# Kernel optimization log

Hardware: AMD Instinct MI355X
Metric: run time of the kernel (lower is better)

## Reference

```python
import jax, jax.numpy as jnp
import numpy as np

E = 1024      # embed_dim
H = 16        # num_heads
HD = E // H   # head_dim = 64
WIN = 256     # window_size
LN_EPS = 1e-5


def _layernorm(x, g, b):
    mu = jnp.mean(x, axis=-1, keepdims=True)
    var = jnp.var(x, axis=-1, keepdims=True)
    return (x - mu) * jax.lax.rsqrt(var + LN_EPS) * g + b


def _rope_tables(S):
    freqs = 1.0 / (10000.0 ** (jnp.arange(0, HD, 2, dtype=jnp.float32) / HD))  # [HD/2]
    t = jnp.arange(S, dtype=jnp.float32)
    fr = jnp.outer(t, freqs)                      # [S, HD/2]
    emb = jnp.concatenate([fr, fr], axis=-1)      # [S, HD]
    # shape [S, 1, HD] so it broadcasts over the heads dim of [B, S, H, HD]
    return emb[:, None, :].astype(jnp.float32), None


def _rotate_half(x):
    x1, x2 = jnp.split(x, 2, axis=-1)
    return jnp.concatenate([-x2, x1], axis=-1)


def setup_inputs() -> dict:
    key = jax.random.key(0)
    ks = jax.random.split(key, 12)
    B, S = 8, 1024
    sc = 0.02
    return {
        "x": jax.random.normal(ks[0], (B, S, E), dtype=jnp.float32),
        "in_proj_w": jax.random.normal(ks[1], (3 * E, E), dtype=jnp.float32) * sc,
        "in_proj_b": jnp.zeros((3 * E,), dtype=jnp.float32),
        "out_proj_w": jax.random.normal(ks[2], (E, E), dtype=jnp.float32) * sc,
        "out_proj_b": jnp.zeros((E,), dtype=jnp.float32),
        "ln1_g": jnp.ones((E,), dtype=jnp.float32),
        "ln1_b": jnp.zeros((E,), dtype=jnp.float32),
        "w1": jax.random.normal(ks[3], (4 * E, E), dtype=jnp.float32) * sc,
        "b1": jnp.zeros((4 * E,), dtype=jnp.float32),
        "w2": jax.random.normal(ks[4], (E, 4 * E), dtype=jnp.float32) * sc,
        "b2": jnp.zeros((E,), dtype=jnp.float32),
        "ln2_g": jnp.ones((E,), dtype=jnp.float32),
        "ln2_b": jnp.zeros((E,), dtype=jnp.float32),
    }


def reference(x, in_proj_w, in_proj_b, out_proj_w, out_proj_b,
              ln1_g, ln1_b, w1, b1, w2, b2, ln2_g, ln2_b):
    B, S, _ = x.shape
    # RoPE applied to the raw input (pre in_proj), as in the torch module
    emb, _ = _rope_tables(S)
    cos, sin = jnp.cos(emb), jnp.sin(emb)          # [S, 1, HD]
    xh = x.reshape(B, S, H, HD)
    roped = xh * cos + _rotate_half(xh) * sin      # [B, S, H, HD]
    qk_in = roped.reshape(B, S, E)

    Wq, Wk, Wv = jnp.split(in_proj_w, 3, axis=0)   # each [E, E]
    bq, bk, bv = jnp.split(in_proj_b, 3, axis=0)
    q = (qk_in @ Wq.T + bq).reshape(B, S, H, HD).transpose(0, 2, 1, 3)  # [B,H,S,HD]
    k = (qk_in @ Wk.T + bk).reshape(B, S, H, HD).transpose(0, 2, 1, 3)
    v = (x @ Wv.T + bv).reshape(B, S, H, HD).transpose(0, 2, 1, 3)

    scale = 1.0 / np.sqrt(HD)
    scores = jnp.einsum("bhqd,bhkd->bhqk", q, k) * scale  # [B,H,S,S]
    idx = jnp.arange(S)
    disallowed = jnp.abs(idx[:, None] - idx[None, :]) > WIN  # [S,S] bool
    scores = jnp.where(disallowed, jnp.float32(-jnp.inf), scores)
    attn = jax.nn.softmax(scores, axis=-1)
    ctx = jnp.einsum("bhqk,bhkd->bhqd", attn, v)            # [B,H,S,HD]
    ctx = ctx.transpose(0, 2, 1, 3).reshape(B, S, E)
    h = ctx @ out_proj_w.T + out_proj_b

    x1 = _layernorm(x + h, ln1_g, ln1_b)
    ff = jax.nn.gelu(x1 @ w1.T + b1, approximate=False) @ w2.T + b2
    return _layernorm(x1 + ff, ln2_g, ln2_b)
```

## Files before the change

kernel.cpp:

```cpp
#include <hip/hip_runtime.h>
#include <stdint.h>


#define B_ 8
#define S_ 1024
#define E_ 1024
#define H_ 16
#define HD_ 64
#define WIN_ 256
#define QKV_ 3072

typedef __attribute__((ext_vector_type(8))) short short8;
typedef __attribute__((ext_vector_type(4))) float f32x4;
typedef __attribute__((ext_vector_type(4))) unsigned short us4;
typedef unsigned short ushort_t;

__device__ __forceinline__ ushort_t f2b(float f) {
  unsigned int u = __builtin_bit_cast(unsigned int, f);
  u = (u + 0x7fffu + ((u >> 16) & 1u)) >> 16;
  return (ushort_t)u;
}

__device__ __forceinline__ ushort_t f2b_trunc(float f) {
  return (ushort_t)(__builtin_bit_cast(unsigned int, f) >> 16);
}

__device__ __forceinline__ float b2f(ushort_t u) {
  return __builtin_bit_cast(float, ((unsigned int)u) << 16);
}

__device__ __forceinline__ float fast_exp2(float x) {
#if __has_builtin(__builtin_amdgcn_exp2f)
  return __builtin_amdgcn_exp2f(x);
#else
  return exp2f(x);
#endif
}

__device__ __forceinline__ float fast_rcp(float x) {
#if __has_builtin(__builtin_amdgcn_rcpf)
  return __builtin_amdgcn_rcpf(x);
#else
  return 1.f / x;
#endif
}

__device__ __forceinline__ void gld_lds16(const void* g, void* l) {
  __builtin_amdgcn_global_load_lds((const __attribute__((address_space(1))) void*)g,
                                   (__attribute__((address_space(3))) void*)l, 16, 0, 0);
}

__global__ __launch_bounds__(256) void cast4_kernel(const float* __restrict__ i0,
                                                    const float* __restrict__ i1,
                                                    const float* __restrict__ i2,
                                                    const float* __restrict__ i3,
                                                    ushort_t* __restrict__ o0,
                                                    ushort_t* __restrict__ o1,
                                                    ushort_t* __restrict__ o2,
                                                    ushort_t* __restrict__ o3) {
  int i = blockIdx.x * 256 + threadIdx.x;
  const float* in;
  ushort_t* out;
  int j;
  if (i < 786432)       { in = i0; out = o0; j = i; }
  else if (i < 1048576) { in = i1; out = o1; j = i - 786432; }
  else if (i < 2097152) { in = i2; out = o2; j = i - 1048576; }
  else                  { in = i3; out = o3; j = i - 2097152; }
  float4 v = ((const float4*)in)[j];
  us4 o;
  o.x = f2b(v.x); o.y = f2b(v.y); o.z = f2b(v.z); o.w = f2b(v.w);
  ((us4*)out)[j] = o;
}

__global__ __launch_bounds__(256) void rope_kernel(const float* __restrict__ x,
                                                   ushort_t* __restrict__ roped,
                                                   ushort_t* __restrict__ xbf) {
  int idx = blockIdx.x * 256 + threadIdx.x;
  int d = idx & 31;
  int h = (idx >> 5) & 15;
  int s = (idx >> 9) & 1023;
  int b = idx >> 19;
  size_t base = ((size_t)(b * S_ + s)) * E_ + h * HD_ + d;
  float x0 = x[base], x1 = x[base + 32];
  float freq = exp2f(-(float)d * 0.41524101186092029f);
  float th = (float)s * freq;
  float sn, cs;
  sincosf(th, &sn, &cs);
  roped[base]      = f2b(x0 * cs - x1 * sn);
  roped[base + 32] = f2b(x1 * cs + x0 * sn);
  xbf[base]      = f2b(x0);
  xbf[base + 32] = f2b(x1);
}

template <int MODE>
__global__ __launch_bounds__(256) void gemm_bt(const ushort_t* __restrict__ A,
                                               const ushort_t* __restrict__ A2,
                                               int nsplit,
                                               const ushort_t* __restrict__ Bm,
                                               const float* __restrict__ bias,
                                               ushort_t* __restrict__ C,
                                               int N, int K) {
  __shared__ ushort_t sA[128 * 64];
  __shared__ ushort_t sB[128 * 64];
  const int tid = threadIdx.x;
  const int lane = tid & 63;
  const int wave = tid >> 6;
  const int quad = lane >> 4;
  const int lq = lane & 15;
  const int wm = (wave & 1) * 64;
  const int wn = (wave >> 1) * 64;
  const size_t bm = (size_t)blockIdx.x * 128;
  const size_t bn = (size_t)blockIdx.y * 128;
  const ushort_t* Asel = (bn >= (size_t)nsplit) ? A2 : A;

  f32x4 acc[4][4] = {};

  const int srow = lane >> 3;
  const int skc = ((lane & 7) ^ (lane >> 3)) * 8;

  for (int k0 = 0; k0 < K; k0 += 64) {
#pragma unroll
    for (int i = 0; i < 4; i++) {
      const int r0 = wave * 32 + i * 8;
      gld_lds16(Asel + (bm + r0 + srow) * K + k0 + skc, &sA[r0 * 64]);
      gld_lds16(Bm + (bn + r0 + srow) * K + k0 + skc, &sB[r0 * 64]);
    }
    __syncthreads();

#pragma unroll
    for (int kk = 0; kk < 2; kk++) {
      const int csw = (((kk * 4) + quad) ^ (lq & 7)) * 8;
      short8 av[4], bv[4];
#pragma unroll
      for (int mt = 0; mt < 4; mt++)
        av[mt] = *(const short8*)&sA[(wm + mt * 16 + lq) * 64 + csw];
#pragma unroll
      for (int nt = 0; nt < 4; nt++)
        bv[nt] = *(const short8*)&sB[(wn + nt * 16 + lq) * 64 + csw];
#pragma unroll
      for (int mt = 0; mt < 4; mt++)
#pragma unroll
        for (int nt = 0; nt < 4; nt++)
          acc[mt][nt] = __builtin_amdgcn_mfma_f32_16x16x32_bf16(av[mt], bv[nt], acc[mt][nt], 0, 0, 0);
    }
    __syncthreads();
  }

#pragma unroll
  for (int mt = 0; mt < 4; mt++) {
#pragma unroll
    for (int nt = 0; nt < 4; nt++) {
      size_t row = bm + wm + mt * 16 + quad * 4;
      size_t col = bn + wn + nt * 16 + lq;
      float bc = bias[col];
#pragma unroll
      for (int r = 0; r < 4; r++) {
        float v = acc[mt][nt][r] + bc;
        if (MODE == 1) {
          float y = 0.7978845608028654f * (v + 0.044715f * v * v * v);
          float t = fast_exp2(y * 2.8853900817779268f);
          v = v * (t * fast_rcp(1.f + t));
        }
        C[(row + r) * N + col] = f2b(v);
      }
    }
  }
}

#define FENCE asm volatile("" ::: "memory")
#define VM6 asm volatile("s_waitcnt vmcnt(6)" ::: "memory")
#define VM0 asm volatile("s_waitcnt vmcnt(0)" ::: "memory")
#define NOPW ((void)0)

#define STAGE_A(bufc, half, kb)                                               \
  { gld_lds16(aSrc + (size_t)((half) * 128) * K + (kb),                       \
              &lds[16384 * (bufc) + 8192 * (half) + wave * 512]);             \
    gld_lds16(aSrc + (size_t)((half) * 128 + 64) * K + (kb),                  \
              &lds[16384 * (bufc) + 8192 * (half) + 4096 + wave * 512]); }

#define STAGE_B(bufc, half, kb)                                               \
  { gld_lds16(bSrc + (size_t)((half) * 128) * K + (kb),                       \
              &lds[32768 + 16384 * (bufc) + 8192 * (half) + wave * 512]);     \
    gld_lds16(bSrc + (size_t)((half) * 128 + 64) * K + (kb),                  \
              &lds[32768 + 16384 * (bufc) + 8192 * (half) + 4096 + wave * 512]); }

#define PHASE(qq, bufc, doA, doB, STAGE_STMT, WAIT_STMT)                      \
  {                                                                           \
    if (doA) {                                                                \
      const int abase = 16384 * (bufc) + 8192 * ((qq) >> 1);                  \
      _Pragma("unroll") for (int mf = 0; mf < 4; mf++) {                      \
        const int ra = wm * 64 + mf * 16 + lq;                                \
        _Pragma("unroll") for (int k2 = 0; k2 < 2; k2++)                      \
          av[mf][k2] = *(const short8*)&lds[abase + ra * 64 +                 \
                                            (((k2 * 4 + quad) ^ (lq & 7)) << 3)]; \
      }                                                                       \
    }                                                                         \
    if (doB) {                                                                \
      const int bbase = 32768 + 16384 * (bufc) +                              \
                        8192 * ((((qq) == 1) || ((qq) == 2)) ? 1 : 0);        \
      _Pragma("unroll") for (int nf = 0; nf < 2; nf++) {                      \
        const int rb = wn * 32 + nf * 16 + lq;                                \
        _Pragma("unroll") for (int k2 = 0; k2 < 2; k2++)                      \
          bv[nf][k2] = *(const short8*)&lds[bbase + rb * 64 +                 \
                                            (((k2 * 4 + quad) ^ (lq & 7)) << 3)]; \
      }                                                                       \
    }                                                                         \
    STAGE_STMT;                                                               \
    FENCE; __builtin_amdgcn_s_barrier(); FENCE;                               \
    __builtin_amdgcn_s_setprio(1);                                            \
    _Pragma("unroll") for (int k2 = 0; k2 < 2; k2++)                          \
      _Pragma("unroll") for (int mf = 0; mf < 4; mf++)                        \
        _Pragma("unroll") for (int nf = 0; nf < 2; nf++)                      \
          acc[qq][mf][nf] = __builtin_amdgcn_mfma_f32_16x16x32_bf16(          \
              av[mf][k2], bv[nf][k2], acc[qq][mf][nf], 0, 0, 0);              \
    __builtin_amdgcn_s_setprio(0);                                            \
    WAIT_STMT;                                                                \
    FENCE; __builtin_amdgcn_s_barrier(); FENCE;                               \
  }

template <int MODE>
__global__ __launch_bounds__(512, 2) void gemm256(const ushort_t* __restrict__ A,
                                                  const ushort_t* __restrict__ A2,
                                                  int nsplit,
                                                  const ushort_t* __restrict__ Bm,
                                                  const float* __restrict__ bias,
                                                  ushort_t* __restrict__ C,
                                                  int N, int K, int nbx) {
  __shared__ ushort_t lds[65536];
  const int tid = threadIdx.x;
  const int lane = tid & 63, wave = tid >> 6;
  const int quad = lane >> 4, lq = lane & 15;
  const int wm = wave >> 2, wn = wave & 3;

  const int nwg = gridDim.x;
  const int id = blockIdx.x;
  const int wg = (nwg & 7) ? id : ((id & 7) * (nwg >> 3) + (id >> 3));
  const int bx = wg % nbx, by = wg / nbx;
  const size_t bm = (size_t)bx * 256, bn = (size_t)by * 256;
  const ushort_t* Asel = ((int)bn >= nsplit) ? A2 : A;

  const int srow = lane >> 3;
  const int scol = ((lane & 7) ^ srow) << 3;
  const ushort_t* aSrc = Asel + (bm + wave * 8 + srow) * (size_t)K + scol;
  const ushort_t* bSrc = Bm + (bn + wave * 8 + srow) * (size_t)K + scol;

  f32x4 acc[4][4][2] = {};
  short8 av[4][2], bv[2][2];

  STAGE_A(0, 0, 0); STAGE_A(0, 1, 0); STAGE_B(0, 0, 0); STAGE_B(0, 1, 0);
  STAGE_A(1, 0, 64); STAGE_B(1, 1, 64); STAGE_A(1, 1, 64);
  VM6;
  FENCE; __builtin_amdgcn_s_barrier(); FENCE;

  const int NT = K >> 6;
#pragma unroll 1
  for (int i = 0; i < (NT >> 1) - 1; i++) {
    const int kb0 = i << 7;
    PHASE(0, 0, 1, 1, STAGE_B(1, 0, kb0 + 64), NOPW);
    PHASE(1, 0, 0, 1, STAGE_A(0, 0, kb0 + 128), NOPW);
    PHASE(2, 0, 1, 0, STAGE_B(0, 1, kb0 + 128), NOPW);
    PHASE(3, 0, 0, 1, STAGE_A(0, 1, kb0 + 128), VM6);
    PHASE(0, 1, 1, 1, STAGE_B(0, 0, kb0 + 128), NOPW);
    PHASE(1, 1, 0, 1, STAGE_A(1, 0, kb0 + 192), NOPW);
    PHASE(2, 1, 1, 0, STAGE_B(1, 1, kb0 + 192), NOPW);
    PHASE(3, 1, 0, 1, STAGE_A(1, 1, kb0 + 192), VM6);
  }
  {
    const int kb0 = (NT - 2) << 6;
    PHASE(0, 0, 1, 1, STAGE_B(1, 0, kb0 + 64), NOPW);
    PHASE(1, 0, 0, 1, NOPW, NOPW);
    PHASE(2, 0, 1, 0, NOPW, NOPW);
    PHASE(3, 0, 0, 1, NOPW, VM0);
    PHASE(0, 1, 1, 1, NOPW, NOPW);
    PHASE(1, 1, 0, 1, NOPW, NOPW);
    PHASE(2, 1, 1, 0, NOPW, NOPW);
    PHASE(3, 1, 0, 1, NOPW, NOPW);
  }

#pragma unroll
  for (int q = 0; q < 4; q++) {
    const int Mh = q >> 1;
    const int Nh = (q == 1 || q == 2) ? 1 : 0;
#pragma unroll
    for (int mf = 0; mf < 4; mf++) {
#pragma unroll
      for (int nf = 0; nf < 2; nf++) {
        size_t row = bm + Mh * 128 + wm * 64 + mf * 16 + quad * 4;
        size_t col = bn + Nh * 128 + wn * 32 + nf * 16 + lq;
        float bc = bias[col];
#pragma unroll
        for (int r = 0; r < 4; r++) {
          float v = acc[q][mf][nf][r] + bc;
          if (MODE == 1) {
            float y = 0.7978845608028654f * (v + 0.044715f * v * v * v);
            float t = fast_exp2(y * 2.8853900817779268f);
            v = v * (t * fast_rcp(1.f + t));
          }
          C[(row + r) * N + col] = f2b(v);
        }
      }
    }
  }
}

__global__ __launch_bounds__(256) void vtrans_kernel(const ushort_t* __restrict__ qkv,
                                                     ushort_t* __restrict__ vt) {
  __shared__ ushort_t tb[64 * 65];
  int bh = blockIdx.x >> 4;
  int st = blockIdx.x & 15;
  int b = bh >> 4, h = bh & 15;
  int s0 = st * 64;
  int tid = threadIdx.x;
  int c = tid & 63, rbase = tid >> 6;
#pragma unroll
  for (int rep = 0; rep < 16; rep++) {
    int i = rep * 4 + rbase;
    tb[c * 65 + i] = qkv[(size_t)(b * S_ + s0 + i) * QKV_ + 2048 + h * HD_ + c];
  }
  __syncthreads();
#pragma unroll
  for (int rep = 0; rep < 16; rep++) {
    int d = rep * 4 + rbase;
    vt[(size_t)((b * H_ + h) * HD_ + d) * S_ + s0 + c] = tb[d * 65 + c];
  }
}

#define SC_ 0.18033688011112042f

__global__ __launch_bounds__(256) void attn_kernel(const ushort_t* __restrict__ qkv,
                                                   const ushort_t* __restrict__ vt,
                                                   ushort_t* __restrict__ ctx) {
  __shared__ ushort_t sK[2][32 * 64];
  __shared__ ushort_t sV[2][64 * 32];
  __shared__ ushort_t sP[4][16 * 36];
  const int tid = threadIdx.x;
  const int lane = tid & 63, wave = tid >> 6;
  const int quad = lane >> 4, lq = lane & 15;
  int gid = ((blockIdx.x & 7) << 8) | (blockIdx.x >> 3);
  int qs = gid & 15;
  int h = (gid >> 4) & 15;
  int b = gid >> 8;
  int qs64 = qs * 64;
  int q0 = qs64 + wave * 16;

  const size_t qoff = (size_t)(b * S_ + q0 + lq) * QKV_ + h * HD_;
  short8 a0 = *(const short8*)&qkv[qoff + quad * 8];
  short8 a1 = *(const short8*)&qkv[qoff + 32 + quad * 8];

  f32x4 o[4] = {};
  float rs[4] = {0.f, 0.f, 0.f, 0.f};

  int start = qs64 - WIN_; if (start < 0) start = 0;
  int end = qs64 + 64 + WIN_; if (end > S_) end = S_;
  const int wlo = q0 - WIN_;
  const int whi = q0 + 16 + WIN_;

  const ushort_t* kg = qkv + (size_t)(b * S_) * QKV_ + 1024 + h * HD_;
  const ushort_t* vg = vt + (size_t)((b * H_ + h) * HD_) * S_;

  const int krow = lane >> 3;
  const int kchg = ((lane & 7) ^ krow) << 3;
  const int vrow = lane >> 2;
  const int vchg = ((lane & 3) ^ ((lane >> 3) & 3)) << 3;

  gld_lds16(kg + (size_t)(start + wave * 8 + krow) * QKV_ + kchg, &sK[0][wave * 512]);
  gld_lds16(vg + (size_t)(wave * 16 + vrow) * S_ + start + vchg, &sV[0][wave * 512]);

  const int nch = (end - start) >> 5;
  int buf = 0;
  for (int c = 0; c < nch; c++) {
    __syncthreads();
    int kb = start + c * 32;
    if (c + 1 < nch) {
      int nkb = kb + 32;
      gld_lds16(kg + (size_t)(nkb + wave * 8 + krow) * QKV_ + kchg, &sK[buf ^ 1][wave * 512]);
      gld_lds16(vg + (size_t)(wave * 16 + vrow) * S_ + nkb + vchg, &sV[buf ^ 1][wave * 512]);
    }
    if (kb < whi && kb + 32 > wlo) {
      f32x4 s[2];
#pragma unroll
      for (int t = 0; t < 2; t++) {
        const ushort_t* kr = &sK[buf][(t * 16 + lq) * 64];
        short8 b0 = *(const short8*)&kr[((quad ^ (lq & 7)) << 3)];
        short8 b1 = *(const short8*)&kr[(((4 + quad) ^ (lq & 7)) << 3)];
        f32x4 z = {};
        z = __builtin_amdgcn_mfma_f32_16x16x32_bf16(a0, b0, z, 0, 0, 0);
        z = __builtin_amdgcn_mfma_f32_16x16x32_bf16(a1, b1, z, 0, 0, 0);
        s[t] = z;
      }
      float p[2][4];
      const bool full = (kb >= q0 - 241) && (kb <= q0 + 225);
      if (full) {
#pragma unroll
        for (int t = 0; t < 2; t++)
#pragma unroll
          for (int r = 0; r < 4; r++) p[t][r] = fast_exp2(s[t][r] * SC_);
      } else {
#pragma unroll
        for (int t = 0; t < 2; t++) {
          int ki = kb + t * 16 + lq;
#pragma unroll
          for (int r = 0; r < 4; r++) {
            int dd = q0 + quad * 4 + r - ki;
            bool allowed = (dd <= WIN_) && (dd >= -WIN_);
            p[t][r] = allowed ? fast_exp2(s[t][r] * SC_) : 0.f;
          }
        }
      }
#pragma unroll
      for (int r = 0; r < 4; r++) rs[r] += p[0][r] + p[1][r];

#pragma unroll
      for (int t = 0; t < 2; t++)
#pragma unroll
        for (int r = 0; r < 4; r++)
          sP[wave][(quad * 4 + r) * 36 + t * 16 + lq] = f2b_trunc(p[t][r]);
      asm volatile("s_waitcnt lgkmcnt(0)" ::: "memory");
      short8 ap = *(const short8*)&sP[wave][lq * 36 + quad * 8];

#pragma unroll
      for (int nt = 0; nt < 4; nt++) {
        short8 bvf = *(const short8*)&sV[buf][(nt * 16 + lq) * 32 +
                                             ((quad ^ ((lq >> 1) & 3)) << 3)];
        o[nt] = __builtin_amdgcn_mfma_f32_16x16x32_bf16(ap, bvf, o[nt], 0, 0, 0);
      }
    }
    buf ^= 1;
  }

  float inv[4];
#pragma unroll
  for (int r = 0; r < 4; r++) {
    float v = rs[r];
    v += __shfl_xor(v, 1);
    v += __shfl_xor(v, 2);
    v += __shfl_xor(v, 4);
    v += __shfl_xor(v, 8);
    inv[r] = 1.f / v;
  }

#pragma unroll
  for (int nt = 0; nt < 4; nt++)
#pragma unroll
    for (int r = 0; r < 4; r++) {
      int row = q0 + quad * 4 + r;
      int col = h * HD_ + nt * 16 + lq;
      ctx[(size_t)(b * S_ + row) * E_ + col] = f2b(o[nt][r] * inv[r]);
    }
}

__global__ __launch_bounds__(256) void ln_res_kernel(const float* __restrict__ A,
                                                     const ushort_t* __restrict__ Bv,
                                                     const float* __restrict__ g,
                                                     const float* __restrict__ be,
                                                     float* __restrict__ outf,
                                                     ushort_t* __restrict__ outb) {
  const int row = blockIdx.x;
  const int tid = threadIdx.x;
  const size_t base = (size_t)row * 1024;
  float4 a4 = ((const float4*)(A + base))[tid];
  us4 b4 = ((const us4*)(Bv + base))[tid];
  float v[4];
  v[0] = a4.x + b2f(b4.x);
  v[1] = a4.y + b2f(b4.y);
  v[2] = a4.z + b2f(b4.z);
  v[3] = a4.w + b2f(b4.w);
  float s = v[0] + v[1] + v[2] + v[3];
  float sq = v[0] * v[0] + v[1] * v[1] + v[2] * v[2] + v[3] * v[3];
#pragma unroll
  for (int off = 32; off; off >>= 1) {
    s += __shfl_xor(s, off);
    sq += __shfl_xor(sq, off);
  }
  __shared__ float ls[4], lsq[4];
  int wave = tid >> 6, lane = tid & 63;
  if (lane == 0) { ls[wave] = s; lsq[wave] = sq; }
  __syncthreads();
  s = ls[0] + ls[1] + ls[2] + ls[3];
  sq = lsq[0] + lsq[1] + lsq[2] + lsq[3];
  float mean = s * (1.f / 1024.f);
  float var = sq * (1.f / 1024.f) - mean * mean;
  float rstd = rsqrtf(var + 1e-5f);
  float4 g4 = ((const float4*)g)[tid];
  float4 e4 = ((const float4*)be)[tid];
  float o0 = (v[0] - mean) * rstd * g4.x + e4.x;
  float o1 = (v[1] - mean) * rstd * g4.y + e4.y;
  float o2 = (v[2] - mean) * rstd * g4.z + e4.z;
  float o3 = (v[3] - mean) * rstd * g4.w + e4.w;
  float4 of = {o0, o1, o2, o3};
  ((float4*)(outf + base))[tid] = of;
  if (outb) {
    us4 ob;
    ob.x = f2b(o0); ob.y = f2b(o1); ob.z = f2b(o2); ob.w = f2b(o3);
    ((us4*)(outb + base))[tid] = ob;
  }
}

#define O_XBF   ((size_t)0)
#define O_ROPED ((size_t)16777216)
#define O_W_IN  ((size_t)33554432)
#define O_W_OUT ((size_t)39845888)
#define O_W1    ((size_t)41943040)
#define O_W2    ((size_t)50331648)
#define O_BIG   ((size_t)58720256)
#define O_VT    ((size_t)125829120)
#define O_X1F   ((size_t)142606336)
#define O_FF2   ((size_t)176160768)

extern "C" void kernel_launch(void* const* d_in, const int* in_sizes, int n_in,
                              void* d_out, int out_size, void* d_ws, size_t ws_size,
                              hipStream_t stream) {
  const float* x          = (const float*)d_in[0];
  const float* in_proj_w  = (const float*)d_in[1];
  const float* in_proj_b  = (const float*)d_in[2];
  const float* out_proj_w = (const float*)d_in[3];
  const float* out_proj_b = (const float*)d_in[4];
  const float* ln1_g      = (const float*)d_in[5];
  const float* ln1_b      = (const float*)d_in[6];
  const float* w1         = (const float*)d_in[7];
  const float* b1         = (const float*)d_in[8];
  const float* w2         = (const float*)d_in[9];
  const float* b2         = (const float*)d_in[10];
  const float* ln2_g      = (const float*)d_in[11];
  const float* ln2_b      = (const float*)d_in[12];
  float* out = (float*)d_out;

  char* ws = (char*)d_ws;
  ushort_t* xbf     = (ushort_t*)(ws + O_XBF);
  ushort_t* roped   = (ushort_t*)(ws + O_ROPED);
  ushort_t* wbf_in  = (ushort_t*)(ws + O_W_IN);
  ushort_t* wbf_out = (ushort_t*)(ws + O_W_OUT);
  ushort_t* wbf_1   = (ushort_t*)(ws + O_W1);
  ushort_t* wbf_2   = (ushort_t*)(ws + O_W2);
  ushort_t* qkv_buf = (ushort_t*)(ws + O_BIG);
  ushort_t* vtb     = (ushort_t*)(ws + O_VT);
  ushort_t* ctx     = (ushort_t*)(ws + O_ROPED);
  ushort_t* h_bf    = (ushort_t*)(ws + O_BIG);
  float*    x1f     = (float*)(ws + O_X1F);
  ushort_t* x1bf    = (ushort_t*)(ws + O_XBF);
  ushort_t* ff1     = (ushort_t*)(ws + O_BIG);
  ushort_t* ff2     = (ushort_t*)(ws + O_FF2);

  dim3 blk(256);
  dim3 blk512(512);
  const int NOSPLIT = 1 << 30;

  cast4_kernel<<<dim3(12288), blk, 0, stream>>>(in_proj_w, out_proj_w, w1, w2,
                                                wbf_in, wbf_out, wbf_1, wbf_2);

  rope_kernel<<<dim3(16384), blk, 0, stream>>>(x, roped, xbf);

  gemm256<0><<<dim3(384), blk512, 0, stream>>>(roped, xbf, 2048, wbf_in, in_proj_b,
                                               qkv_buf, QKV_, 1024, 32);
  vtrans_kernel<<<dim3(2048), blk, 0, stream>>>(qkv_buf, vtb);

  attn_kernel<<<dim3(2048), blk, 0, stream>>>(qkv_buf, vtb, ctx);

  gemm_bt<0><<<dim3(64, 8), blk, 0, stream>>>(ctx, ctx, NOSPLIT, wbf_out, out_proj_b,
                                              h_bf, 1024, 1024);

  ln_res_kernel<<<dim3(8192), blk, 0, stream>>>(x, h_bf, ln1_g, ln1_b, x1f, x1bf);

  gemm256<1><<<dim3(512), blk512, 0, stream>>>(x1bf, x1bf, NOSPLIT, wbf_1, b1,
                                               ff1, 4096, 1024, 32);

  gemm_bt<0><<<dim3(64, 8), blk, 0, stream>>>(ff1, ff1, NOSPLIT, wbf_2, b2,
                                              ff2, 1024, 4096);

  ln_res_kernel<<<dim3(8192), blk, 0, stream>>>(x1f, ff2, ln2_g, ln2_b, out, nullptr);
}
```

Before: 455.1 us.

## Split-K the FFN down-projection on the 256-tile GEMM and fuse partial reduction into LayerNorm

Adds a split-K mode to the 256x256 GEMM kernel. The FFN second projection (K=4096, N=1024) now runs as 256 workgroups, each doing half of K, and writes fp32 partial sums to two buffers instead of using the smaller gemm_bt kernel. A new LayerNorm kernel sums the residual, both partials and the bias before normalising, which replaces the bf16 ff2 intermediate. The aim is to fill the GPU with the faster large-tile GEMM. The cost is extra fp32 write and read traffic for the partials, and the bias pointer is reused to carry the second partial buffer.

```diff
diff --git a/kernel.cpp b/kernel.cpp
--- a/kernel.cpp
+++ b/kernel.cpp
@@ -225,7 +225,8 @@
                                                   const ushort_t* __restrict__ Bm,
                                                   const float* __restrict__ bias,
                                                   ushort_t* __restrict__ C,
-                                                  int N, int K, int nbx) {
+                                                  int N, int Klen, int K,
+                                                  int nbx, int nbn) {
   __shared__ ushort_t lds[65536];
   const int tid = threadIdx.x;
   const int lane = tid & 63, wave = tid >> 6;
@@ -235,14 +236,18 @@
   const int nwg = gridDim.x;
   const int id = blockIdx.x;
   const int wg = (nwg & 7) ? id : ((id & 7) * (nwg >> 3) + (id >> 3));
-  const int bx = wg % nbx, by = wg / nbx;
-  const size_t bm = (size_t)bx * 256, bn = (size_t)by * 256;
+  const int bx = wg % nbx;
+  const int byt = wg / nbx;
+  const int bny = byt % nbn;
+  const int ks = byt / nbn;
+  const size_t bm = (size_t)bx * 256, bn = (size_t)bny * 256;
   const ushort_t* Asel = ((int)bn >= nsplit) ? A2 : A;
+  const size_t koff = (size_t)ks * Klen;
 
   const int srow = lane >> 3;
   const int scol = ((lane & 7) ^ srow) << 3;
-  const ushort_t* aSrc = Asel + (bm + wave * 8 + srow) * (size_t)K + scol;
-  const ushort_t* bSrc = Bm + (bn + wave * 8 + srow) * (size_t)K + scol;
+  const ushort_t* aSrc = Asel + (bm + wave * 8 + srow) * (size_t)K + koff + scol;
+  const ushort_t* bSrc = Bm + (bn + wave * 8 + srow) * (size_t)K + koff + scol;
 
   f32x4 acc[4][4][2] = {};
   short8 av[4][2], bv[2][2];
@@ -252,7 +257,7 @@
   VM6;
   FENCE; __builtin_amdgcn_s_barrier(); FENCE;
 
-  const int NT = K >> 6;
+  const int NT = Klen >> 6;
 #pragma unroll 1
   for (int i = 0; i < (NT >> 1) - 1; i++) {
     const int kb0 = i << 7;
@@ -277,6 +282,7 @@
     PHASE(3, 1, 0, 1, NOPW, NOPW);
   }
 
+  float* Pf = (MODE == 2) ? (ks ? (float*)bias : (float*)C) : nullptr;
 #pragma unroll
   for (int q = 0; q < 4; q++) {
     const int Mh = q >> 1;
@@ -287,7 +293,7 @@
       for (int nf = 0; nf < 2; nf++) {
         size_t row = bm + Mh * 128 + wm * 64 + mf * 16 + quad * 4;
         size_t col = bn + Nh * 128 + wn * 32 + nf * 16 + lq;
-        float bc = bias[col];
+        float bc = (MODE == 2) ? 0.f : bias[col];
 #pragma unroll
         for (int r = 0; r < 4; r++) {
           float v = acc[q][mf][nf][r] + bc;
@@ -296,7 +302,11 @@
             float t = fast_exp2(y * 2.8853900817779268f);
             v = v * (t * fast_rcp(1.f + t));
           }
-          C[(row + r) * N + col] = f2b(v);
+          if (MODE == 2) {
+            Pf[(row + r) * (size_t)N + col] = v;
+          } else {
+            C[(row + r) * N + col] = f2b(v);
+          }
         }
       }
     }
@@ -496,6 +506,51 @@
   }
 }
 
+__global__ __launch_bounds__(256) void ln_res2_kernel(const float* __restrict__ A,
+                                                      const float* __restrict__ P0,
+                                                      const float* __restrict__ P1,
+                                                      const float* __restrict__ bias,
+                                                      const float* __restrict__ g,
+                                                      const float* __restrict__ be,
+                                                      float* __restrict__ outf) {
+  const int row = blockIdx.x;
+  const int tid = threadIdx.x;
+  const size_t base = (size_t)row * 1024;
+  float4 a4 = ((const float4*)(A + base))[tid];
+  float4 p04 = ((const float4*)(P0 + base))[tid];
+  float4 p14 = ((const float4*)(P1 + base))[tid];
+  float4 bi4 = ((const float4*)bias)[tid];
+  float v[4];
+  v[0] = a4.x + p04.x + p14.x + bi4.x;
+  v[1] = a4.y + p04.y + p14.y + bi4.y;
+  v[2] = a4.z + p04.z + p14.z + bi4.z;
+  v[3] = a4.w + p04.w + p14.w + bi4.w;
+  float s = v[0] + v[1] + v[2] + v[3];
+  float sq = v[0] * v[0] + v[1] * v[1] + v[2] * v[2] + v[3] * v[3];
+#pragma unroll
+  for (int off = 32; off; off >>= 1) {
+    s += __shfl_xor(s, off);
+    sq += __shfl_xor(sq, off);
+  }
+  __shared__ float ls[4], lsq[4];
+  int wave = tid >> 6, lane = tid & 63;
+  if (lane == 0) { ls[wave] = s; lsq[wave] = sq; }
+  __syncthreads();
+  s = ls[0] + ls[1] + ls[2] + ls[3];
+  sq = lsq[0] + lsq[1] + lsq[2] + lsq[3];
+  float mean = s * (1.f / 1024.f);
+  float var = sq * (1.f / 1024.f) - mean * mean;
+  float rstd = rsqrtf(var + 1e-5f);
+  float4 g4 = ((const float4*)g)[tid];
+  float4 e4 = ((const float4*)be)[tid];
+  float4 of;
+  of.x = (v[0] - mean) * rstd * g4.x + e4.x;
+  of.y = (v[1] - mean) * rstd * g4.y + e4.y;
+  of.z = (v[2] - mean) * rstd * g4.z + e4.z;
+  of.w = (v[3] - mean) * rstd * g4.w + e4.w;
+  ((float4*)(outf + base))[tid] = of;
+}
+
 #define O_XBF   ((size_t)0)
 #define O_ROPED ((size_t)16777216)
 #define O_W_IN  ((size_t)33554432)
@@ -505,7 +560,7 @@
 #define O_BIG   ((size_t)58720256)
 #define O_VT    ((size_t)125829120)
 #define O_X1F   ((size_t)142606336)
-#define O_FF2   ((size_t)176160768)
+#define O_P1    ((size_t)176160768)
 
 extern "C" void kernel_launch(void* const* d_in, const int* in_sizes, int n_in,
                               void* d_out, int out_size, void* d_ws, size_t ws_size,
@@ -539,7 +594,8 @@
   float*    x1f     = (float*)(ws + O_X1F);
   ushort_t* x1bf    = (ushort_t*)(ws + O_XBF);
   ushort_t* ff1     = (ushort_t*)(ws + O_BIG);
-  ushort_t* ff2     = (ushort_t*)(ws + O_FF2);
+  float*    p0      = (float*)(ws + O_XBF);
+  float*    p1      = (float*)(ws + O_P1);
 
   dim3 blk(256);
   dim3 blk512(512);
@@ -551,7 +607,7 @@
   rope_kernel<<<dim3(16384), blk, 0, stream>>>(x, roped, xbf);
 
   gemm256<0><<<dim3(384), blk512, 0, stream>>>(roped, xbf, 2048, wbf_in, in_proj_b,
-                                               qkv_buf, QKV_, 1024, 32);
+                                               qkv_buf, QKV_, 1024, 1024, 32, 12);
   vtrans_kernel<<<dim3(2048), blk, 0, stream>>>(qkv_buf, vtb);
 
   attn_kernel<<<dim3(2048), blk, 0, stream>>>(qkv_buf, vtb, ctx);
@@ -562,10 +618,11 @@
   ln_res_kernel<<<dim3(8192), blk, 0, stream>>>(x, h_bf, ln1_g, ln1_b, x1f, x1bf);
 
   gemm256<1><<<dim3(512), blk512, 0, stream>>>(x1bf, x1bf, NOSPLIT, wbf_1, b1,
-                                               ff1, 4096, 1024, 32);
-
-  gemm_bt<0><<<dim3(64, 8), blk, 0, stream>>>(ff1, ff1, NOSPLIT, wbf_2, b2,
-                                              ff2, 1024, 4096);
-
-  ln_res_kernel<<<dim3(8192), blk, 0, stream>>>(x1f, ff2, ln2_g, ln2_b, out, nullptr);
-}
+                                               ff1, 4096, 1024, 1024, 32, 16);
+
+  gemm256<2><<<dim3(256), blk512, 0, stream>>>(ff1, ff1, NOSPLIT, wbf_2,
+                                               (const float*)p1, (ushort_t*)p0,
+                                               1024, 2048, 4096, 32, 4);
+
+  ln_res2_kernel<<<dim3(8192), blk, 0, stream>>>(x1f, p0, p1, b2, ln2_g, ln2_b, out);
+}
```

Result: slower. 471.4 us (+3.6%).
